# Performance work log

Measured on AMD Instinct MI355X. Metric: run time of the kernel, lower is better.

Reference implementation:

```python
import jax, jax.numpy as jnp
import numpy as np

B, IN, H, MID = 16384, 256, 512, 64
GRID_SIZE, ORDER = 5, 3
GRID_LO, GRID_HI = -1.0, 1.0
NB = GRID_SIZE + ORDER  # 8 spline basis functions per input feature
LN_EPS = 1e-5


def make_grid(in_features):
    h = (GRID_HI - GRID_LO) / GRID_SIZE
    g = np.arange(-ORDER, GRID_SIZE + ORDER + 1, dtype=np.float32) * h + GRID_LO
    return jnp.asarray(np.tile(g, (in_features, 1)))  # (in, grid_size + 2*order + 1)


def layer_norm(x, g, b):
    mu = jnp.mean(x, axis=-1, keepdims=True)
    var = jnp.var(x, axis=-1, keepdims=True)
    return (x - mu) * jax.lax.rsqrt(var + LN_EPS) * g + b


def b_splines(x, grid):
    # x: (B, in), grid: (in, G). Cox-de Boor recursion (efficient-kan convention).
    xe = x[:, :, None]
    bases = ((xe >= grid[:, :-1]) & (xe < grid[:, 1:])).astype(x.dtype)
    for k in range(1, ORDER + 1):
        left = (xe - grid[:, :-(k + 1)]) / (grid[:, k:-1] - grid[:, :-(k + 1)])
        right = (grid[:, k + 1:] - xe) / (grid[:, k + 1:] - grid[:, 1:-k])
        bases = left * bases[:, :, :-1] + right * bases[:, :, 1:]
    return bases  # (B, in, NB)


def kan_linear(x, base_w, spline_w, scaler, grid):
    # base path: silu(x) @ W_base^T ; spline path: B-spline bases contracted with scaled spline weights
    base = jax.nn.silu(x) @ base_w.T
    bs = b_splines(x, grid)
    spline = jnp.einsum('bik,oik->bo', bs, spline_w * scaler[:, :, None])
    return base + spline


def setup_inputs() -> dict:
    key = jax.random.key(0)
    ks = jax.random.split(key, 24)

    def n(k, shape, fan_in):
        return jax.random.normal(k, shape, dtype=jnp.float32) / np.sqrt(fan_in)

    H2 = 2 * H
    return {
        'x': jax.random.normal(ks[0], (B, IN), jnp.float32),
        'h_prev': jax.random.normal(ks[1], (B, H), jnp.float32),
        'ip_w': n(ks[2], (H, IN), IN), 'ip_b': jnp.zeros((H,), jnp.float32),
        'rg_w': n(ks[3], (H, H2), H2), 'rg_b': jnp.zeros((H,), jnp.float32),
        'rg_g': jnp.ones((H,), jnp.float32), 'rg_beta': jnp.zeros((H,), jnp.float32),
        'ug_w': n(ks[4], (H, H2), H2), 'ug_b': jnp.zeros((H,), jnp.float32),
        'ug_g': jnp.ones((H,), jnp.float32), 'ug_beta': jnp.zeros((H,), jnp.float32),
        'k1_base': n(ks[5], (MID, H2), H2),
        'k1_spline': n(ks[6], (MID, H2, NB), H2) * 0.1,
        'k1_scaler': n(ks[7], (MID, H2), H2) + 1.0,
        'grid1': make_grid(H2),
        'k2_base': n(ks[8], (H, MID), MID),
        'k2_spline': n(ks[9], (H, MID, NB), MID) * 0.1,
        'k2_scaler': n(ks[10], (H, MID), MID) + 1.0,
        'grid2': make_grid(MID),
        'cn_g': jnp.ones((H,), jnp.float32), 'cn_b': jnp.zeros((H,), jnp.float32),
        'rp_w': n(ks[11], (H, H2), H2), 'rp_b': jnp.zeros((H,), jnp.float32),
    }


def reference(x, h_prev, ip_w, ip_b, rg_w, rg_b, rg_g, rg_beta, ug_w, ug_b, ug_g, ug_beta,
              k1_base, k1_spline, k1_scaler, grid1, k2_base, k2_spline, k2_scaler, grid2,
              cn_g, cn_b, rp_w, rp_b):
    x_proj = x @ ip_w.T + ip_b
    combined = jnp.concatenate([x_proj, h_prev], axis=1)  # (B, 2H)
    # reset gate is computed in the original forward but never used; kept for faithfulness
    reset = jnp.tanh(layer_norm(combined @ rg_w.T + rg_b, rg_g, rg_beta))  # noqa: F841
    update = jax.nn.sigmoid(layer_norm(combined @ ug_w.T + ug_b, ug_g, ug_beta))
    # KAN candidate: [2H] -> 64 -> H
    mid = kan_linear(combined, k1_base, k1_spline, k1_scaler, grid1)
    h_cand = kan_linear(mid, k2_base, k2_spline, k2_scaler, grid2)
    residual = combined @ rp_w.T + rp_b
    h_cand = layer_norm(h_cand + residual, cn_g, cn_b)
    h_cand = layer_norm(h_cand, cn_g, cn_b)  # same LayerNorm applied twice, as in source
    h_cand = jax.nn.silu(h_cand)
    h_t = (1.0 - update) * h_prev + update * h_cand
    return h_t
```

## Files before the change

kernel.cpp:

```cpp
#include <hip/hip_runtime.h>
#include <hip/hip_bf16.h>

#define BATCH 16384

typedef __attribute__((ext_vector_type(8))) short short8;
typedef __attribute__((ext_vector_type(4))) float f32x4;

typedef const __attribute__((address_space(1))) uint* gas_t;
typedef __attribute__((address_space(3))) uint* las_t;

__device__ __forceinline__ void gl_lds16(const void* g, void* l) {
    __builtin_amdgcn_global_load_lds((gas_t)g, (las_t)l, 16, 0, 0);
}

__device__ __forceinline__ float bf2f(uint u) { union { uint u; float f; } v; v.u = u << 16; return v.f; }
__device__ __forceinline__ ushort f2bf(float f) {
    union { float f; uint u; } v; v.f = f;
    uint r = v.u + 0x7fffu + ((v.u >> 16) & 1u);
    return (ushort)(r >> 16);
}
__device__ __forceinline__ uint pack2(float a, float b) { return (uint)f2bf(a) | ((uint)f2bf(b) << 16); }
__device__ __forceinline__ uint pack_trunc(float lo, float hi) {
    return __builtin_amdgcn_perm(__float_as_uint(hi), __float_as_uint(lo), 0x07060302u);
}
__device__ __forceinline__ float sigmoidf_(float x) { return __builtin_amdgcn_rcpf(1.0f + __expf(-x)); }
__device__ __forceinline__ float siluf_(float x)    { return x * sigmoidf_(x); }

__device__ __forceinline__ void bases_packed(float x, float g0, float inv_h, uint o[4]) {
    float u = (x - g0) * inv_h;
    float fl = floorf(u);
    float f = u - fl;
    float f2 = f * f, f3 = f2 * f;
    float Ca = f3 * (1.0f / 6.0f);
    float Cb = (1.0f / 6.0f) + 0.5f * (f + f2 - f3);
    float Cc = (2.0f / 3.0f) + 0.5f * f3 - f2;
    float Cd = (1.0f / 6.0f) + 0.5f * (f2 - f) - f3 * (1.0f / 6.0f);
    int t0 = (int)fl;
    t0 = max(-8, min(t0, 19));
    uint dlo = pack_trunc(Cd, Cc);
    uint dhi = pack_trunc(Cb, Ca);
    unsigned long long D = (unsigned long long)dlo | ((unsigned long long)dhi << 32);
    int sp = t0 * 16 - 48;
    unsigned long long l1 = D << (sp & 63);
    unsigned long long r1 = D >> ((-sp) & 63);
    unsigned long long r2 = D >> ((64 - sp) & 63);
    unsigned long long l2 = D << ((sp - 64) & 63);
    unsigned long long lo = (sp >= 0) ? (sp < 64 ? l1 : 0ull) : (sp > -64 ? r1 : 0ull);
    unsigned long long hi = (sp > 0 && sp < 128) ? (sp < 64 ? r2 : l2) : 0ull;
    o[0] = (uint)lo; o[1] = (uint)(lo >> 32); o[2] = (uint)hi; o[3] = (uint)(hi >> 32);
}

__device__ __forceinline__ short8 bases_frag(float x, float g0, float inv_h) {
    uint o[4];
    bases_packed(x, g0, inv_h, o);
    union { uint4 u; short8 s; } v;
    v.u.x = o[0]; v.u.y = o[1]; v.u.z = o[2]; v.u.w = o[3];
    return v.s;
}

__device__ __forceinline__ short8 silu_frag(uint4 raw) {
    uint rr[4] = {raw.x, raw.y, raw.z, raw.w};
    union { uint4 u; short8 s; } v;
    uint oo[4];
#pragma unroll
    for (int p = 0; p < 4; ++p) {
        float lo = siluf_(bf2f(rr[p] & 0xffffu));
        float hi = siluf_(bf2f(rr[p] >> 16));
        oo[p] = pack_trunc(lo, hi);
    }
    v.u.x = oo[0]; v.u.y = oo[1]; v.u.z = oo[2]; v.u.w = oo[3];
    return v.s;
}

__global__ __launch_bounds__(256) void prep_all(const float* __restrict__ ip_w, const float* __restrict__ ug_w,
                                                const float* __restrict__ rp,  const float* __restrict__ k2b,
                                                const float* __restrict__ k2s, const float* __restrict__ k2sc,
                                                const float* __restrict__ k1b, const float* __restrict__ k1s,
                                                const float* __restrict__ k1sc,
                                                ushort* __restrict__ ipw, ushort* __restrict__ ugw,
                                                ushort* __restrict__ wcat, ushort* __restrict__ w1aug) {
    int t = blockIdx.x * 256 + threadIdx.x;
    if (t < 131072) { ipw[t] = f2bf(ip_w[t]); return; }
    t -= 131072;
    if (t < 524288) { ugw[t] = f2bf(ug_w[t]); return; }
    t -= 524288;
    if (t < 819200) {
        int n = t / 1600, c = t % 1600; float v;
        if (c < 1024) v = rp[n * 1024 + c];
        else if (c < 1088) v = k2b[n * 64 + (c - 1024)];
        else { int i = (c - 1088) >> 3, k = (c - 1088) & 7; v = k2s[(n * 64 + i) * 8 + k] * k2sc[n * 64 + i]; }
        wcat[t] = f2bf(v); return;
    }
    t -= 819200;
    if (t < 589824) {
        int n = t / 9216, r = t % 9216;
        int klog = (r & ~63) | ((((r >> 3) & 7) ^ (n & 7)) << 3) | (r & 7);
        float v;
        if (klog < 1024) v = k1b[n * 1024 + klog];
        else { int i = (klog - 1024) >> 3, k = (klog - 1024) & 7; v = k1s[(n * 1024 + i) * 8 + k] * k1sc[n * 1024 + i]; }
        w1aug[t] = f2bf(v);
    }
}

__global__ __launch_bounds__(256) void copy_h_bf(const float* __restrict__ hp, ushort* __restrict__ acat) {
    int t = blockIdx.x * 256 + threadIdx.x;
    int b = t >> 6, j = (t & 63) * 8;
    const float4* s = (const float4*)(hp + (size_t)b * 512 + j);
    float4 a = s[0], c = s[1];
    uint4 o; o.x = pack2(a.x, a.y); o.y = pack2(a.z, a.w); o.z = pack2(c.x, c.y); o.w = pack2(c.z, c.w);
    *(uint4*)(acat + (size_t)b * 1600 + 512 + j) = o;
}

__global__ __launch_bounds__(256) void gemm_mfma(const ushort* __restrict__ A, int lda,
                                                 const ushort* __restrict__ Wt, int ldw,
                                                 const float* __restrict__ bias,
                                                 ushort* __restrict__ C, int ldc, int K) {
    __shared__ ushort As[2][128 * 64];
    __shared__ ushort Bs[2][128 * 64];
    const int tid = threadIdx.x;
    const int w = tid >> 6, lane = tid & 63;
    const int fr = lane & 15, fq = lane >> 4;
    const int m0 = blockIdx.x * 128, n0 = blockIdx.y * 128;
    const int wm = w & 1, wn = w >> 1;

    const int srow8 = lane >> 3;
    const int scol  = ((lane & 7) ^ srow8) << 3;
    const ushort* gA[4]; const ushort* gB[4]; int fa[4];
#pragma unroll
    for (int j = 0; j < 4; ++j) {
        int rowj = (j * 4 + w) * 8 + srow8;
        fa[j] = (j * 4 + w) * 512 + lane * 8;
        gA[j] = A  + (size_t)(m0 + rowj) * lda + scol;
        gB[j] = Wt + (size_t)(n0 + rowj) * ldw + scol;
    }
    const int nt = K / 64;
#pragma unroll
    for (int j = 0; j < 4; ++j) {
        gl_lds16(gA[j], &As[0][fa[j]]); gl_lds16(gB[j], &Bs[0][fa[j]]);
        gA[j] += 64; gB[j] += 64;
    }
    f32x4 acc[4][4] = {};
    int cur = 0;
    for (int t = 0; t < nt; ++t) {
        __syncthreads();
        if (t + 1 < nt) {
#pragma unroll
            for (int j = 0; j < 4; ++j) {
                gl_lds16(gA[j], &As[cur ^ 1][fa[j]]); gl_lds16(gB[j], &Bs[cur ^ 1][fa[j]]);
                gA[j] += 64; gB[j] += 64;
            }
        }
#pragma unroll
        for (int s = 0; s < 2; ++s) {
            const int csw = ((s * 4 + fq) ^ (fr & 7)) << 3;
            short8 af[4], bv[4];
#pragma unroll
            for (int mi = 0; mi < 4; ++mi)
                af[mi] = *(const short8*)(&As[cur][(wm * 64 + mi * 16 + fr) * 64 + csw]);
#pragma unroll
            for (int ni = 0; ni < 4; ++ni)
                bv[ni] = *(const short8*)(&Bs[cur][(wn * 64 + ni * 16 + fr) * 64 + csw]);
#pragma unroll
            for (int mi = 0; mi < 4; ++mi)
#pragma unroll
                for (int ni = 0; ni < 4; ++ni)
                    acc[mi][ni] = __builtin_amdgcn_mfma_f32_16x16x32_bf16(af[mi], bv[ni], acc[mi][ni], 0, 0, 0);
        }
        cur ^= 1;
    }
#pragma unroll
    for (int mi = 0; mi < 4; ++mi) {
#pragma unroll
        for (int ni = 0; ni < 4; ++ni) {
            int n = n0 + wn * 64 + ni * 16 + fr;
            float bvs = bias[n];
#pragma unroll
            for (int r = 0; r < 4; ++r) {
                int m = m0 + wm * 64 + mi * 16 + fq * 4 + r;
                C[(size_t)m * ldc + n] = f2bf(acc[mi][ni][r] + bvs);
            }
        }
    }
}

__global__ __launch_bounds__(256) void gemm_ip(const float* __restrict__ X,
                                               const ushort* __restrict__ Wt,
                                               const float* __restrict__ bias,
                                               ushort* __restrict__ acat) {
    __shared__ ushort As[2][128 * 64];
    __shared__ ushort Bs[2][128 * 64];
    const int tid = threadIdx.x;
    const int w = tid >> 6, lane = tid & 63;
    const int fr = lane & 15, fq = lane >> 4;
    const int m0 = blockIdx.x * 128, n0 = blockIdx.y * 128;
    const int wm = w & 1, wn = w >> 1;

    const int srow8 = lane >> 3;
    const int scol = ((lane & 7) ^ srow8) << 3;
    const ushort* gB[4]; int fa[4];
#pragma unroll
    for (int j = 0; j < 4; ++j) {
        int rowj = (j * 4 + w) * 8 + srow8;
        fa[j] = (j * 4 + w) * 512 + lane * 8;
        gB[j] = Wt + (size_t)(n0 + rowj) * 256 + scol;
    }
    const float* gA[4]; int ar[4];
#pragma unroll
    for (int j = 0; j < 4; ++j) {
        int rj = j * 32 + (tid >> 3);
        int lc = (tid & 7) ^ (rj & 7);
        ar[j] = rj * 64 + (tid & 7) * 8;
        gA[j] = X + (size_t)(m0 + rj) * 256 + lc * 8;
    }
    float4 va[4], vb[4];
#pragma unroll
    for (int j = 0; j < 4; ++j) { gl_lds16(gB[j], &Bs[0][fa[j]]); gB[j] += 64; }
#pragma unroll
    for (int j = 0; j < 4; ++j) { va[j] = *(const float4*)gA[j]; vb[j] = *(const float4*)(gA[j] + 4); gA[j] += 64; }
#pragma unroll
    for (int j = 0; j < 4; ++j) {
        uint4 o; o.x = pack2(va[j].x, va[j].y); o.y = pack2(va[j].z, va[j].w);
        o.z = pack2(vb[j].x, vb[j].y); o.w = pack2(vb[j].z, vb[j].w);
        *(uint4*)&As[0][ar[j]] = o;
    }
    f32x4 acc[4][4] = {};
    int cur = 0;
    for (int t = 0; t < 4; ++t) {
        __syncthreads();
        if (t < 3) {
#pragma unroll
            for (int j = 0; j < 4; ++j) { gl_lds16(gB[j], &Bs[cur ^ 1][fa[j]]); gB[j] += 64; }
#pragma unroll
            for (int j = 0; j < 4; ++j) { va[j] = *(const float4*)gA[j]; vb[j] = *(const float4*)(gA[j] + 4); gA[j] += 64; }
        }
#pragma unroll
        for (int s = 0; s < 2; ++s) {
            const int csw = ((s * 4 + fq) ^ (fr & 7)) << 3;
            short8 af[4], bv[4];
#pragma unroll
            for (int mi = 0; mi < 4; ++mi)
                af[mi] = *(const short8*)(&As[cur][(wm * 64 + mi * 16 + fr) * 64 + csw]);
#pragma unroll
            for (int ni = 0; ni < 4; ++ni)
                bv[ni] = *(const short8*)(&Bs[cur][(wn * 64 + ni * 16 + fr) * 64 + csw]);
#pragma unroll
            for (int mi = 0; mi < 4; ++mi)
#pragma unroll
                for (int ni = 0; ni < 4; ++ni)
                    acc[mi][ni] = __builtin_amdgcn_mfma_f32_16x16x32_bf16(af[mi], bv[ni], acc[mi][ni], 0, 0, 0);
        }
        if (t < 3) {
#pragma unroll
            for (int j = 0; j < 4; ++j) {
                uint4 o; o.x = pack2(va[j].x, va[j].y); o.y = pack2(va[j].z, va[j].w);
                o.z = pack2(vb[j].x, vb[j].y); o.w = pack2(vb[j].z, vb[j].w);
                *(uint4*)&As[cur ^ 1][ar[j]] = o;
            }
        }
        cur ^= 1;
    }
#pragma unroll
    for (int mi = 0; mi < 4; ++mi) {
#pragma unroll
        for (int ni = 0; ni < 4; ++ni) {
            int n = n0 + wn * 64 + ni * 16 + fr;
            float bvs = bias[n];
#pragma unroll
            for (int r = 0; r < 4; ++r) {
                int m = m0 + wm * 64 + mi * 16 + fq * 4 + r;
                acat[(size_t)m * 1600 + n] = f2bf(acc[mi][ni][r] + bvs);
            }
        }
    }
}

__global__ __launch_bounds__(256) void kan1_mfma(const ushort* __restrict__ acat,
                                                 const ushort* __restrict__ w1aug,
                                                 const float* __restrict__ grid1,
                                                 float* __restrict__ midp) {
    __shared__ ushort Bs[2][64 * 64];
    const int tid = threadIdx.x;
    const int wid = tid >> 6, lane = tid & 63;
    const int fr = lane & 15, fq = lane >> 4;
    const int m0 = blockIdx.x * 128;
    const int kb = blockIdx.y;
    const float g0 = grid1[0];
    const float inv_h = 1.0f / (grid1[1] - g0);

    const ushort* aRow0 = acat + (size_t)(m0 + wid * 32 + fr) * 1600;
    const ushort* aRow1 = acat + (size_t)(m0 + wid * 32 + 16 + fr) * 1600;

    const int brow = tid >> 3, bpc = tid & 7;
    const ushort* gB0 = w1aug + (size_t)brow * 9216 + bpc * 8;
    const ushort* gB1 = w1aug + (size_t)(brow + 32) * 9216 + bpc * 8;

#define KCOL(s) ((s) < 16 ? 1024 + kb * 1024 + (s) * 64 : kb * 128 + ((s) - 16) * 64)

    f32x4 acc[2][4] = {};
    short8 afc[2][2], afn[2][2];
    uint  xp[2][2][2];
    uint4 sc[2][2][2];

    const int xoff = kb * 128 + fq;

    gl_lds16(gB0 + KCOL(0), &Bs[0][tid * 8]);
    gl_lds16(gB1 + KCOL(0), &Bs[0][2048 + tid * 8]);
    xp[0][0][0] = aRow0[xoff];       xp[0][0][1] = aRow0[xoff + 4];
    xp[0][1][0] = aRow1[xoff];       xp[0][1][1] = aRow1[xoff + 4];
    xp[1][0][0] = aRow0[xoff + 8];   xp[1][0][1] = aRow0[xoff + 12];
    xp[1][1][0] = aRow1[xoff + 8];   xp[1][1][1] = aRow1[xoff + 12];
#pragma unroll
    for (int mi = 0; mi < 2; ++mi)
#pragma unroll
        for (int s2 = 0; s2 < 2; ++s2)
            afc[mi][s2] = bases_frag(bf2f(xp[0][mi][s2]), g0, inv_h);
    __syncthreads();

#pragma unroll
    for (int s = 0; s < 18; ++s) {
        const int cur = s & 1;
        if (s + 1 < 18) {
            gl_lds16(gB0 + KCOL(s + 1), &Bs[cur ^ 1][tid * 8]);
            gl_lds16(gB1 + KCOL(s + 1), &Bs[cur ^ 1][2048 + tid * 8]);
        }
        if (s + 2 < 16) {
            const int xo = xoff + (s + 2) * 8;
            xp[s & 1][0][0] = aRow0[xo];     xp[s & 1][0][1] = aRow0[xo + 4];
            xp[s & 1][1][0] = aRow1[xo];     xp[s & 1][1][1] = aRow1[xo + 4];
        } else if (s + 2 < 18) {
            const int col = KCOL(s + 2) + fq * 8;
            sc[s & 1][0][0] = *(const uint4*)(aRow0 + col);
            sc[s & 1][0][1] = *(const uint4*)(aRow0 + col + 32);
            sc[s & 1][1][0] = *(const uint4*)(aRow1 + col);
            sc[s & 1][1][1] = *(const uint4*)(aRow1 + col + 32);
        }
#pragma unroll
        for (int s2 = 0; s2 < 2; ++s2) {
#pragma unroll
            for (int ni = 0; ni < 4; ++ni) {
                const int row = ni * 16 + fr;
                short8 bv = *(const short8*)(&Bs[cur][row * 64 + (((s2 * 4 + fq) ^ (row & 7)) << 3)]);
                acc[0][ni] = __builtin_amdgcn_mfma_f32_16x16x32_bf16(afc[0][s2], bv, acc[0][ni], 0, 0, 0);
                acc[1][ni] = __builtin_amdgcn_mfma_f32_16x16x32_bf16(afc[1][s2], bv, acc[1][ni], 0, 0, 0);
            }
        }
        if (s + 1 < 16) {
#pragma unroll
            for (int mi = 0; mi < 2; ++mi)
#pragma unroll
                for (int s2 = 0; s2 < 2; ++s2)
                    afn[mi][s2] = bases_frag(bf2f(xp[(s + 1) & 1][mi][s2]), g0, inv_h);
        } else if (s + 1 < 18) {
#pragma unroll
            for (int mi = 0; mi < 2; ++mi)
#pragma unroll
                for (int s2 = 0; s2 < 2; ++s2)
                    afn[mi][s2] = silu_frag(sc[(s + 1) & 1][mi][s2]);
        }
#pragma unroll
        for (int mi = 0; mi < 2; ++mi)
#pragma unroll
            for (int s2 = 0; s2 < 2; ++s2) afc[mi][s2] = afn[mi][s2];
        __syncthreads();
    }
#undef KCOL

    float* outp = midp + (size_t)kb * (BATCH * 64);
#pragma unroll
    for (int mi = 0; mi < 2; ++mi)
#pragma unroll
        for (int ni = 0; ni < 4; ++ni)
#pragma unroll
            for (int r = 0; r < 4; ++r)
                outp[(size_t)(m0 + wid * 32 + mi * 16 + fq * 4 + r) * 64 + ni * 16 + fr] = acc[mi][ni][r];
}

__global__ __launch_bounds__(256) void bs2_kernel(const float* __restrict__ midp,
                                                  const float* __restrict__ grid2,
                                                  ushort* __restrict__ acat) {
    int t = blockIdx.x * 256 + threadIdx.x;
    if (t >= BATCH * 64) return;
    float x = 0.0f;
#pragma unroll
    for (int p = 0; p < 8; ++p) x += midp[(size_t)p * (BATCH * 64) + t];
    int b = t >> 6, i = t & 63;
    float g0 = grid2[0], inv_h = 1.0f / (grid2[1] - g0);
    acat[(size_t)b * 1600 + 1024 + i] = f2bf(siluf_(x));
    uint o[4];
    bases_packed(x, g0, inv_h, o);
    uint4 o4; o4.x = o[0]; o4.y = o[1]; o4.z = o[2]; o4.w = o[3];
    *(uint4*)&acat[(size_t)b * 1600 + 1088 + i * 8] = o4;
}

__device__ __forceinline__ void block_reduce_2(float& a, float& b, float (*red)[4]) {
#pragma unroll
    for (int off = 32; off; off >>= 1) {
        a += __shfl_xor(a, off, 64);
        b += __shfl_xor(b, off, 64);
    }
    int lane = threadIdx.x & 63, wid = threadIdx.x >> 6;
    if (lane == 0) { red[0][wid] = a; red[1][wid] = b; }
    __syncthreads();
    a = red[0][0] + red[0][1] + red[0][2] + red[0][3];
    b = red[1][0] + red[1][1] + red[1][2] + red[1][3];
}

__global__ __launch_bounds__(256) void final2(const ushort* __restrict__ ug,
                                              const ushort* __restrict__ hcb,
                                              const ushort* __restrict__ acat,
                                              const float* __restrict__ ug_g,
                                              const float* __restrict__ ug_beta,
                                              const float* __restrict__ cg,
                                              const float* __restrict__ cb,
                                              float* __restrict__ out) {
    int row = blockIdx.x, tid = threadIdx.x;
    __shared__ float rA[2][4], rB[2][4], rC[2][4];
    float u0 = bf2f((uint)ug[(size_t)row * 512 + tid]);
    float u1 = bf2f((uint)ug[(size_t)row * 512 + tid + 256]);
    float h0 = bf2f((uint)hcb[(size_t)row * 512 + tid]);
    float h1 = bf2f((uint)hcb[(size_t)row * 512 + tid + 256]);
    float hp0 = bf2f((uint)acat[(size_t)row * 1600 + 512 + tid]);
    float hp1 = bf2f((uint)acat[(size_t)row * 1600 + 768 + tid]);
    float s = u0 + u1, ss = u0 * u0 + u1 * u1;
    block_reduce_2(s, ss, rA);
    float mu = s * (1.0f / 512.0f);
    float var = ss * (1.0f / 512.0f) - mu * mu;
    float r = rsqrtf(var + 1e-5f);
    float uu0 = sigmoidf_((u0 - mu) * r * ug_g[tid] + ug_beta[tid]);
    float uu1 = sigmoidf_((u1 - mu) * r * ug_g[tid + 256] + ug_beta[tid + 256]);
    float cg0 = cg[tid], cg1 = cg[tid + 256], cb0 = cb[tid], cb1 = cb[tid + 256];
    float s2 = h0 + h1, ss2 = h0 * h0 + h1 * h1;
    block_reduce_2(s2, ss2, rB);
    float mu2 = s2 * (1.0f / 512.0f);
    float var2 = ss2 * (1.0f / 512.0f) - mu2 * mu2;
    float r2 = rsqrtf(var2 + 1e-5f);
    float w0 = (h0 - mu2) * r2 * cg0 + cb0;
    float w1 = (h1 - mu2) * r2 * cg1 + cb1;
    float s3 = w0 + w1, ss3 = w0 * w0 + w1 * w1;
    block_reduce_2(s3, ss3, rC);
    float mu3 = s3 * (1.0f / 512.0f);
    float var3 = ss3 * (1.0f / 512.0f) - mu3 * mu3;
    float r3 = rsqrtf(var3 + 1e-5f);
    float c0 = siluf_((w0 - mu3) * r3 * cg0 + cb0);
    float c1 = siluf_((w1 - mu3) * r3 * cg1 + cb1);
    size_t o0 = (size_t)row * 512 + tid, o1 = o0 + 256;
    out[o0] = (1.0f - uu0) * hp0 + uu0 * c0;
    out[o1] = (1.0f - uu1) * hp1 + uu1 * c1;
}

extern "C" void kernel_launch(void* const* d_in, const int* in_sizes, int n_in,
                              void* d_out, int out_size, void* d_ws, size_t ws_size,
                              hipStream_t stream) {
    const float* x        = (const float*)d_in[0];
    const float* h_prev   = (const float*)d_in[1];
    const float* ip_w     = (const float*)d_in[2];
    const float* ip_b     = (const float*)d_in[3];
    const float* ug_w     = (const float*)d_in[8];
    const float* ug_b     = (const float*)d_in[9];
    const float* ug_g     = (const float*)d_in[10];
    const float* ug_beta  = (const float*)d_in[11];
    const float* k1_base  = (const float*)d_in[12];
    const float* k1_spline= (const float*)d_in[13];
    const float* k1_scaler= (const float*)d_in[14];
    const float* grid1    = (const float*)d_in[15];
    const float* k2_base  = (const float*)d_in[16];
    const float* k2_spline= (const float*)d_in[17];
    const float* k2_scaler= (const float*)d_in[18];
    const float* grid2    = (const float*)d_in[19];
    const float* cn_g     = (const float*)d_in[20];
    const float* cn_b     = (const float*)d_in[21];
    const float* rp_w     = (const float*)d_in[22];
    const float* rp_b     = (const float*)d_in[23];
    float* out = (float*)d_out;
    char* W = (char*)d_ws;

    ushort* Acat    = (ushort*)(W);
    ushort* ug_bf   = (ushort*)(W + 52428800);
    float*  midp    = (float*) (W + 69206016);
    ushort* hc_bf   = (ushort*)(W + 102760448);
    ushort* ipw_bf  = (ushort*)(W + 136314880);
    ushort* ugw_bf  = (ushort*)(W + 136577024);
    ushort* wcat    = (ushort*)(W + 137625600);
    ushort* w1aug   = (ushort*)(W + 139264000);

    hipLaunchKernelGGL(prep_all, dim3(8064), dim3(256), 0, stream,
                       ip_w, ug_w, rp_w, k2_base, k2_spline, k2_scaler,
                       k1_base, k1_spline, k1_scaler, ipw_bf, ugw_bf, wcat, w1aug);
    hipLaunchKernelGGL(copy_h_bf, dim3(4096), dim3(256), 0, stream, h_prev, Acat);

    hipLaunchKernelGGL(gemm_ip, dim3(BATCH / 128, 4), dim3(256), 0, stream,
                       x, ipw_bf, ip_b, Acat);

    hipLaunchKernelGGL(gemm_mfma, dim3(BATCH / 128, 4), dim3(256), 0, stream,
                       Acat, 1600, ugw_bf, 1024, ug_b, ug_bf, 512, 1024);

    hipLaunchKernelGGL(kan1_mfma, dim3(BATCH / 128, 8), dim3(256), 0, stream,
                       Acat, w1aug, grid1, midp);
    hipLaunchKernelGGL(bs2_kernel, dim3(BATCH * 64 / 256), dim3(256), 0, stream, midp, grid2, Acat);

    hipLaunchKernelGGL(gemm_mfma, dim3(BATCH / 128, 4), dim3(256), 0, stream,
                       Acat, 1600, wcat, 1600, rp_b, hc_bf, 512, 1600);

    hipLaunchKernelGGL(final2, dim3(BATCH), dim3(256), 0, stream, ug_bf, hc_bf, Acat, ug_g, ug_beta, cn_g, cn_b, out);
}
```

Measured before the change: 170.5 us.

## Restructure KAN1 split-K into nine slices with large LDS weight tiles

The kan1 kernel now splits K into 9 blocks: one block handles the SiLU base path over 1024 columns and eight handle the spline columns. Each block loads a whole 64x512 weight tile into LDS per half, which replaces the per-step double-buffered 64x64 tiles and their per-step barriers. This removes most synchronisation and separates the silu and spline code paths, so fewer branches run per step. In exchange it uses 64 KB of LDS per block, which can reduce occupancy, it no longer overlaps the weight loads with compute, and it adds a ninth partial buffer that bs2 must sum.

```diff
diff --git a/kernel.cpp b/kernel.cpp
--- a/kernel.cpp
+++ b/kernel.cpp
@@ -278,7 +278,7 @@
                                                  const ushort* __restrict__ w1aug,
                                                  const float* __restrict__ grid1,
                                                  float* __restrict__ midp) {
-    __shared__ ushort Bs[2][64 * 64];
+    __shared__ ushort Bs[64 * 512];
     const int tid = threadIdx.x;
     const int wid = tid >> 6, lane = tid & 63;
     const int fr = lane & 15, fq = lane >> 4;
@@ -287,83 +287,71 @@
     const float g0 = grid1[0];
     const float inv_h = 1.0f / (grid1[1] - g0);
 
+    const int kstart = (kb == 0) ? 0 : 1024 + (kb - 1) * 1024;
     const ushort* aRow0 = acat + (size_t)(m0 + wid * 32 + fr) * 1600;
     const ushort* aRow1 = acat + (size_t)(m0 + wid * 32 + 16 + fr) * 1600;
 
-    const int brow = tid >> 3, bpc = tid & 7;
-    const ushort* gB0 = w1aug + (size_t)brow * 9216 + bpc * 8;
-    const ushort* gB1 = w1aug + (size_t)(brow + 32) * 9216 + bpc * 8;
-
-#define KCOL(s) ((s) < 16 ? 1024 + kb * 1024 + (s) * 64 : kb * 128 + ((s) - 16) * 64)
-
     f32x4 acc[2][4] = {};
-    short8 afc[2][2], afn[2][2];
-    uint  xp[2][2][2];
-    uint4 sc[2][2][2];
-
-    const int xoff = kb * 128 + fq;
-
-    gl_lds16(gB0 + KCOL(0), &Bs[0][tid * 8]);
-    gl_lds16(gB1 + KCOL(0), &Bs[0][2048 + tid * 8]);
-    xp[0][0][0] = aRow0[xoff];       xp[0][0][1] = aRow0[xoff + 4];
-    xp[0][1][0] = aRow1[xoff];       xp[0][1][1] = aRow1[xoff + 4];
-    xp[1][0][0] = aRow0[xoff + 8];   xp[1][0][1] = aRow0[xoff + 12];
-    xp[1][1][0] = aRow1[xoff + 8];   xp[1][1][1] = aRow1[xoff + 12];
-#pragma unroll
-    for (int mi = 0; mi < 2; ++mi)
-#pragma unroll
-        for (int s2 = 0; s2 < 2; ++s2)
-            afc[mi][s2] = bases_frag(bf2f(xp[0][mi][s2]), g0, inv_h);
-    __syncthreads();
-
-#pragma unroll
-    for (int s = 0; s < 18; ++s) {
-        const int cur = s & 1;
-        if (s + 1 < 18) {
-            gl_lds16(gB0 + KCOL(s + 1), &Bs[cur ^ 1][tid * 8]);
-            gl_lds16(gB1 + KCOL(s + 1), &Bs[cur ^ 1][2048 + tid * 8]);
-        }
-        if (s + 2 < 16) {
-            const int xo = xoff + (s + 2) * 8;
-            xp[s & 1][0][0] = aRow0[xo];     xp[s & 1][0][1] = aRow0[xo + 4];
-            xp[s & 1][1][0] = aRow1[xo];     xp[s & 1][1][1] = aRow1[xo + 4];
-        } else if (s + 2 < 18) {
-            const int col = KCOL(s + 2) + fq * 8;
-            sc[s & 1][0][0] = *(const uint4*)(aRow0 + col);
-            sc[s & 1][0][1] = *(const uint4*)(aRow0 + col + 32);
-            sc[s & 1][1][0] = *(const uint4*)(aRow1 + col);
-            sc[s & 1][1][1] = *(const uint4*)(aRow1 + col + 32);
-        }
-#pragma unroll
-        for (int s2 = 0; s2 < 2; ++s2) {
-#pragma unroll
-            for (int ni = 0; ni < 4; ++ni) {
-                const int row = ni * 16 + fr;
-                short8 bv = *(const short8*)(&Bs[cur][row * 64 + (((s2 * 4 + fq) ^ (row & 7)) << 3)]);
-                acc[0][ni] = __builtin_amdgcn_mfma_f32_16x16x32_bf16(afc[0][s2], bv, acc[0][ni], 0, 0, 0);
-                acc[1][ni] = __builtin_amdgcn_mfma_f32_16x16x32_bf16(afc[1][s2], bv, acc[1][ni], 0, 0, 0);
-            }
-        }
-        if (s + 1 < 16) {
-#pragma unroll
-            for (int mi = 0; mi < 2; ++mi)
-#pragma unroll
-                for (int s2 = 0; s2 < 2; ++s2)
-                    afn[mi][s2] = bases_frag(bf2f(xp[(s + 1) & 1][mi][s2]), g0, inv_h);
-        } else if (s + 1 < 18) {
-#pragma unroll
-            for (int mi = 0; mi < 2; ++mi)
-#pragma unroll
-                for (int s2 = 0; s2 < 2; ++s2)
-                    afn[mi][s2] = silu_frag(sc[(s + 1) & 1][mi][s2]);
-        }
-#pragma unroll
-        for (int mi = 0; mi < 2; ++mi)
-#pragma unroll
-            for (int s2 = 0; s2 < 2; ++s2) afc[mi][s2] = afn[mi][s2];
+
+#pragma unroll
+    for (int half = 0; half < 2; ++half) {
+        const int ks = kstart + half * 512;
+#pragma unroll
+        for (int L = 0; L < 16; ++L) {
+            const int row = L * 4 + wid;
+            gl_lds16(w1aug + (size_t)row * 9216 + ks + lane * 8,
+                     &Bs[row * 512 + lane * 8]);
+        }
         __syncthreads();
-    }
-#undef KCOL
+
+        if (kb != 0) {
+            const int fbase = (ks - 1024) >> 3;
+            uint xa[16], xb[16];
+#pragma unroll
+            for (int t = 0; t < 16; ++t) {
+                xa[t] = aRow0[fbase + fq + 4 * t];
+                xb[t] = aRow1[fbase + fq + 4 * t];
+            }
+#pragma unroll
+            for (int st = 0; st < 8; ++st) {
+#pragma unroll
+                for (int s2 = 0; s2 < 2; ++s2) {
+                    short8 af0 = bases_frag(bf2f(xa[2 * st + s2]), g0, inv_h);
+                    short8 af1 = bases_frag(bf2f(xb[2 * st + s2]), g0, inv_h);
+#pragma unroll
+                    for (int ni = 0; ni < 4; ++ni) {
+                        const int row = ni * 16 + fr;
+                        short8 bv = *(const short8*)(&Bs[row * 512 + st * 64 + (((s2 * 4 + fq) ^ (row & 7)) << 3)]);
+                        acc[0][ni] = __builtin_amdgcn_mfma_f32_16x16x32_bf16(af0, bv, acc[0][ni], 0, 0, 0);
+                        acc[1][ni] = __builtin_amdgcn_mfma_f32_16x16x32_bf16(af1, bv, acc[1][ni], 0, 0, 0);
+                    }
+                }
+            }
+        } else {
+            uint4 c0 = *(const uint4*)(aRow0 + ks + fq * 8);
+            uint4 c1 = *(const uint4*)(aRow1 + ks + fq * 8);
+#pragma unroll
+            for (int u = 0; u < 16; ++u) {
+                uint4 n0, n1;
+                if (u + 1 < 16) {
+                    n0 = *(const uint4*)(aRow0 + ks + (u + 1) * 32 + fq * 8);
+                    n1 = *(const uint4*)(aRow1 + ks + (u + 1) * 32 + fq * 8);
+                }
+                short8 af0 = silu_frag(c0);
+                short8 af1 = silu_frag(c1);
+                const int st = u >> 1, s2 = u & 1;
+#pragma unroll
+                for (int ni = 0; ni < 4; ++ni) {
+                    const int row = ni * 16 + fr;
+                    short8 bv = *(const short8*)(&Bs[row * 512 + st * 64 + (((s2 * 4 + fq) ^ (row & 7)) << 3)]);
+                    acc[0][ni] = __builtin_amdgcn_mfma_f32_16x16x32_bf16(af0, bv, acc[0][ni], 0, 0, 0);
+                    acc[1][ni] = __builtin_amdgcn_mfma_f32_16x16x32_bf16(af1, bv, acc[1][ni], 0, 0, 0);
+                }
+                c0 = n0; c1 = n1;
+            }
+        }
+        if (half == 0) __syncthreads();
+    }
 
     float* outp = midp + (size_t)kb * (BATCH * 64);
 #pragma unroll
@@ -382,7 +370,7 @@
     if (t >= BATCH * 64) return;
     float x = 0.0f;
 #pragma unroll
-    for (int p = 0; p < 8; ++p) x += midp[(size_t)p * (BATCH * 64) + t];
+    for (int p = 0; p < 9; ++p) x += midp[(size_t)p * (BATCH * 64) + t];
     int b = t >> 6, i = t & 63;
     float g0 = grid2[0], inv_h = 1.0f / (grid2[1] - g0);
     acat[(size_t)b * 1600 + 1024 + i] = f2bf(siluf_(x));
@@ -477,7 +465,7 @@
     ushort* Acat    = (ushort*)(W);
     ushort* ug_bf   = (ushort*)(W + 52428800);
     float*  midp    = (float*) (W + 69206016);
-    ushort* hc_bf   = (ushort*)(W + 102760448);
+    ushort* hc_bf   = (ushort*)(W + 106954752);
     ushort* ipw_bf  = (ushort*)(W + 136314880);
     ushort* ugw_bf  = (ushort*)(W + 136577024);
     ushort* wcat    = (ushort*)(W + 137625600);
@@ -494,7 +482,7 @@
     hipLaunchKernelGGL(gemm_mfma, dim3(BATCH / 128, 4), dim3(256), 0, stream,
                        Acat, 1600, ugw_bf, 1024, ug_b, ug_bf, 512, 1024);
 
-    hipLaunchKernelGGL(kan1_mfma, dim3(BATCH / 128, 8), dim3(256), 0, stream,
+    hipLaunchKernelGGL(kan1_mfma, dim3(BATCH / 128, 9), dim3(256), 0, stream,
                        Acat, w1aug, grid1, midp);
     hipLaunchKernelGGL(bs2_kernel, dim3(BATCH * 64 / 256), dim3(256), 0, stream, midp, grid2, Acat);
 
```

After: 181.3 us. 1.06x slower.
